# Performance work log

Hardware: AMD Instinct MI355X
Metric: run time of the kernel (lower is better)

Reference implementation:

```python
import jax, jax.numpy as jnp
import numpy as np

EPS = 1e-6
DATA_DIM = 2048
LATENT_DIM = 64
ENC = [1024, 1024, 2048]
BATCH = 8192
K_ROUNDS = 24  # fixed proposal rounds for Marsaglia-Tsang rejection (accept prob per round > 0.95)


def _sample_gamma_boosted(key, al, be):
    """Marsaglia-Tsang sampler with alpha-boost, matching the torch al<1 branch.

    Samples Gamma(al+1, 1) via squeeze/rejection, then applies the
    u^(1/al) boost and divides by be, exactly as:
    exp(log(d*v + 1e-6) + log(u + 1e-6)/(al + 1e-6)) / (be + 1e-6)
    """
    d = (al + 1.0) - 1.0 / 3.0              # [B, L]
    c = 1.0 / jnp.sqrt(9.0 * d)             # [B, L]
    k1, k2 = jax.random.split(key)
    eps = jax.random.normal(k1, (K_ROUNDS,) + al.shape, dtype=al.dtype)
    u = jax.random.uniform(k2, (K_ROUNDS,) + al.shape, dtype=al.dtype,
                           minval=1e-7, maxval=1.0)
    v = 1.0 + c[None] * eps                 # [K, B, L]
    v3 = v * v * v
    safe_v3 = jnp.where(v > 0, v3, 1.0)
    # squeeze accept OR full log-accept (standard MT test, as in source index1/index2)
    accept = (v > 0) & ((u < 1.0 - 0.0331 * (eps * eps) * (eps * eps)) |
                        (jnp.log(u) < 0.5 * eps * eps + d[None] * (1.0 - safe_v3 + jnp.log(safe_v3))))
    idx = jnp.argmax(accept, axis=0)        # first accepted round per element
    eps_s = jnp.take_along_axis(eps, idx[None], axis=0)[0]
    u_s = jnp.take_along_axis(u, idx[None], axis=0)[0]
    v_s = (1.0 + c * eps_s) ** 3
    return jnp.exp(jnp.log(d * v_s + EPS) + jnp.log(u_s + EPS) / (al + EPS)) / (be + EPS)


def setup_inputs() -> dict:
    key = jax.random.key(0)
    ks = jax.random.split(key, 20)

    def lin(k, fan_in, fan_out):
        kw, kb = jax.random.split(k)
        w = jax.random.normal(kw, (fan_in, fan_out), dtype=jnp.float32) / np.sqrt(fan_in)
        b = jax.random.normal(kb, (fan_out,), dtype=jnp.float32) * 0.01
        return w, b

    inp = {"x": jax.random.uniform(ks[0], (BATCH, DATA_DIM), dtype=jnp.float32)}
    inp["fc1_w"], inp["fc1_b"] = lin(ks[1], DATA_DIM, ENC[0])
    inp["fc2_w"], inp["fc2_b"] = lin(ks[2], ENC[0], ENC[1])
    inp["fc3_w"], inp["fc3_b"] = lin(ks[3], ENC[1], ENC[2])
    inp["fc41_w"], inp["fc41_b"] = lin(ks[4], ENC[2], LATENT_DIM)
    inp["fc42_w"], inp["fc42_b"] = lin(ks[5], ENC[2], LATENT_DIM)
    inp["fc4_w"], inp["fc4_b"] = lin(ks[6], LATENT_DIM, ENC[2])
    inp["fc5_w"], inp["fc5_b"] = lin(ks[7], ENC[2], ENC[1])
    inp["fc6_w"], inp["fc6_b"] = lin(ks[8], ENC[1], ENC[0])
    inp["fc7_w"], inp["fc7_b"] = lin(ks[9], ENC[0], DATA_DIM * 2)
    return inp


def reference(x, fc1_w, fc1_b, fc2_w, fc2_b, fc3_w, fc3_b,
              fc41_w, fc41_b, fc42_w, fc42_b,
              fc4_w, fc4_b, fc5_w, fc5_b, fc6_w, fc6_b, fc7_w, fc7_b):
    relu, sp = jax.nn.relu, jax.nn.softplus
    # encoder
    h1 = relu(x @ fc1_w + fc1_b)
    h2 = relu(h1 @ fc2_w + fc2_b)
    h3 = relu(h2 @ fc3_w + fc3_b)
    logalpha = EPS + sp(h3 @ fc41_w + fc41_b)   # [B, L], positive
    logbeta = EPS + sp(h3 @ fc42_w + fc42_b)
    # reparameterize via Marsaglia-Tsang gamma rejection sampling
    z = _sample_gamma_boosted(jax.random.key(42), logalpha, logbeta)
    # decoder (torch calls decode(z) twice with identical result; compute once)
    h4 = relu(z @ fc4_w + fc4_b)
    h5 = relu(h4 @ fc5_w + fc5_b)
    h6 = relu(h5 @ fc6_w + fc6_b)
    dec = h6 @ fc7_w + fc7_b                    # [B, 2*DATA_DIM]
    recon_al = EPS + sp(dec[:, :DATA_DIM])
    recon_be = EPS + sp(dec[:, DATA_DIM:])
    return (recon_al, recon_be, logalpha, logbeta, z)
```

## Files before the change

kernel.cpp:

```cpp
#include <hip/hip_runtime.h>
#include <stdint.h>

#define DEVFN static __device__ __forceinline__

typedef __attribute__((ext_vector_type(8))) short short8;
typedef __attribute__((ext_vector_type(4))) float floatx4;
typedef _Float16 half8 __attribute__((ext_vector_type(8)));

DEVFN uint32_t rotl32(uint32_t v, int d) { return (v << d) | (v >> (32 - d)); }

DEVFN void tf2x32(uint32_t k0, uint32_t k1, uint32_t x0, uint32_t x1,
                  uint32_t& o0, uint32_t& o1) {
  uint32_t k2 = k0 ^ k1 ^ 0x1BD11BDAu;
  x0 += k0; x1 += k1;
  x0 += x1; x1 = rotl32(x1, 13); x1 ^= x0;
  x0 += x1; x1 = rotl32(x1, 15); x1 ^= x0;
  x0 += x1; x1 = rotl32(x1, 26); x1 ^= x0;
  x0 += x1; x1 = rotl32(x1, 6);  x1 ^= x0;
  x0 += k1; x1 += k2 + 1u;
  x0 += x1; x1 = rotl32(x1, 17); x1 ^= x0;
  x0 += x1; x1 = rotl32(x1, 29); x1 ^= x0;
  x0 += x1; x1 = rotl32(x1, 16); x1 ^= x0;
  x0 += x1; x1 = rotl32(x1, 24); x1 ^= x0;
  x0 += k2; x1 += k0 + 2u;
  x0 += x1; x1 = rotl32(x1, 13); x1 ^= x0;
  x0 += x1; x1 = rotl32(x1, 15); x1 ^= x0;
  x0 += x1; x1 = rotl32(x1, 26); x1 ^= x0;
  x0 += x1; x1 = rotl32(x1, 6);  x1 ^= x0;
  x0 += k0; x1 += k1 + 3u;
  x0 += x1; x1 = rotl32(x1, 17); x1 ^= x0;
  x0 += x1; x1 = rotl32(x1, 29); x1 ^= x0;
  x0 += x1; x1 = rotl32(x1, 16); x1 ^= x0;
  x0 += x1; x1 = rotl32(x1, 24); x1 ^= x0;
  x0 += k1; x1 += k2 + 4u;
  x0 += x1; x1 = rotl32(x1, 13); x1 ^= x0;
  x0 += x1; x1 = rotl32(x1, 15); x1 ^= x0;
  x0 += x1; x1 = rotl32(x1, 26); x1 ^= x0;
  x0 += x1; x1 = rotl32(x1, 6);  x1 ^= x0;
  x0 += k2; x1 += k0 + 5u;
  o0 = x0; o1 = x1;
}

DEVFN float erfinv_f32(float x) {
#pragma clang fp contract(off)
  float w = -log1pf(-(x * x));
  float p;
  if (w < 5.0f) {
    w = w - 2.5f;
    p = 2.81022636e-08f;
    p = 3.43273939e-07f + p * w;
    p = -3.5233877e-06f + p * w;
    p = -4.39150654e-06f + p * w;
    p = 0.00021858087f + p * w;
    p = -0.00125372503f + p * w;
    p = -0.00417768164f + p * w;
    p = 0.246640727f + p * w;
    p = 1.50140941f + p * w;
  } else {
    w = __fsqrt_rn(w) - 3.0f;
    p = -0.000200214257f;
    p = 0.000100950558f + p * w;
    p = 0.00134934322f + p * w;
    p = -0.00367342844f + p * w;
    p = 0.00573950773f + p * w;
    p = -0.0076224613f + p * w;
    p = 0.00943887047f + p * w;
    p = 1.00167406f + p * w;
    p = 2.83297682f + p * w;
  }
  return p * x;
}

DEVFN float softplus_ref(float v) {
#pragma clang fp contract(off)
  return fmaxf(v, 0.0f) + log1pf(expf(-fabsf(v)));
}

DEVFN ushort f2bf(float f) {
  uint32_t u = __float_as_uint(f);
  uint32_t r = (u + 0x7FFFu + ((u >> 16) & 1u)) >> 16;
  return (ushort)r;
}

DEVFN void split2(float a, ushort& hb, ushort& lb) {
  _Float16 h = (_Float16)a;
  float r = (a - (float)h) * 2048.0f;
  _Float16 l = (_Float16)r;
  hb = __builtin_bit_cast(unsigned short, h);
  lb = __builtin_bit_cast(unsigned short, l);
}

DEVFN void gl2lds16(const void* g, void* l) {
  __builtin_amdgcn_global_load_lds(
      (const __attribute__((address_space(1))) void*)g,
      (__attribute__((address_space(3))) void*)l, 16, 0, 0);
}

__global__ __launch_bounds__(256) void split_f16(
    const float* __restrict__ in, ushort* __restrict__ oh,
    ushort* __restrict__ ol, int n4) {
  int idx = blockIdx.x * 256 + threadIdx.x;
  int stride = gridDim.x * 256;
  for (int i = idx; i < n4; i += stride) {
    float4 a = ((const float4*)in)[i];
    ushort h0, h1, h2, h3, l0, l1, l2, l3;
    split2(a.x, h0, l0); split2(a.y, h1, l1);
    split2(a.z, h2, l2); split2(a.w, h3, l3);
    ushort4 hv; hv.x = h0; hv.y = h1; hv.z = h2; hv.w = h3;
    ushort4 lv; lv.x = l0; lv.y = l1; lv.z = l2; lv.w = l3;
    ((ushort4*)oh)[i] = hv;
    ((ushort4*)ol)[i] = lv;
  }
}

__global__ __launch_bounds__(256) void transpose_split_f16(
    const float* __restrict__ in, ushort* __restrict__ oh,
    ushort* __restrict__ ol, int R, int C) {
  __shared__ float tile[32][33];
  const int c0 = blockIdx.x * 32, r0 = blockIdx.y * 32;
  const int tx = threadIdx.x & 31, ty = threadIdx.x >> 5;
#pragma unroll
  for (int i = ty; i < 32; i += 8)
    tile[i][tx] = in[(size_t)(r0 + i) * C + c0 + tx];
  __syncthreads();
#pragma unroll
  for (int i = ty; i < 32; i += 8) {
    ushort hb, lb;
    split2(tile[tx][i], hb, lb);
    size_t o = (size_t)(c0 + i) * R + r0 + tx;
    oh[o] = hb; ol[o] = lb;
  }
}

template <int ACT>
__global__ __launch_bounds__(256) void gemm_f16x3(
    const ushort* __restrict__ Ah, const ushort* __restrict__ Al,
    const ushort* __restrict__ Bh, const ushort* __restrict__ Bl,
    const float* __restrict__ bias, ushort* __restrict__ Oh,
    ushort* __restrict__ Ol, float* __restrict__ Of, int M, int N, int K) {
  __shared__ ushort AsH[128 * 32];
  __shared__ ushort AsL[128 * 32];
  __shared__ ushort BsH[128 * 32];
  __shared__ ushort BsL[128 * 32];
  const int tid = threadIdx.x;
  const int wave = tid >> 6, lane = tid & 63;
  const int m0 = blockIdx.y * 128, n0 = blockIdx.x * 128;
  const int lrow = lane & 15, lq = lane >> 4;
  const int wm = wave & 1, wn = wave >> 1;
  const int srow = lane >> 2;
  const int scol = (lane & 3) * 8;

  floatx4 acc1[4][4], acc2[4][4];
#pragma unroll
  for (int i = 0; i < 4; i++)
#pragma unroll
    for (int j = 0; j < 4; j++) {
      acc1[i][j] = (floatx4){0.f, 0.f, 0.f, 0.f};
      acc2[i][j] = (floatx4){0.f, 0.f, 0.f, 0.f};
    }

  for (int k0 = 0; k0 < K; k0 += 32) {
#pragma unroll
    for (int h = 0; h < 2; h++) {
      int r0 = wave * 32 + h * 16;
      gl2lds16(Ah + (size_t)(m0 + r0 + srow) * K + k0 + scol, &AsH[r0 * 32]);
      gl2lds16(Al + (size_t)(m0 + r0 + srow) * K + k0 + scol, &AsL[r0 * 32]);
      gl2lds16(Bh + (size_t)(n0 + r0 + srow) * K + k0 + scol, &BsH[r0 * 32]);
      gl2lds16(Bl + (size_t)(n0 + r0 + srow) * K + k0 + scol, &BsL[r0 * 32]);
    }
    __syncthreads();
    half8 ah[4], al[4];
#pragma unroll
    for (int i = 0; i < 4; i++) {
      ah[i] = *(const half8*)&AsH[(wm * 64 + i * 16 + lrow) * 32 + lq * 8];
      al[i] = *(const half8*)&AsL[(wm * 64 + i * 16 + lrow) * 32 + lq * 8];
    }
#pragma unroll
    for (int j = 0; j < 4; j++) {
      half8 bh = *(const half8*)&BsH[(wn * 64 + j * 16 + lrow) * 32 + lq * 8];
      half8 bl = *(const half8*)&BsL[(wn * 64 + j * 16 + lrow) * 32 + lq * 8];
#pragma unroll
      for (int i = 0; i < 4; i++) {
        acc1[i][j] = __builtin_amdgcn_mfma_f32_16x16x32_f16(ah[i], bh,
                                                            acc1[i][j], 0, 0, 0);
        acc2[i][j] = __builtin_amdgcn_mfma_f32_16x16x32_f16(ah[i], bl,
                                                            acc2[i][j], 0, 0, 0);
        acc2[i][j] = __builtin_amdgcn_mfma_f32_16x16x32_f16(al[i], bh,
                                                            acc2[i][j], 0, 0, 0);
      }
    }
    __syncthreads();
  }

  const float INV2048 = 4.8828125e-4f;
#pragma unroll
  for (int i = 0; i < 4; i++) {
#pragma unroll
    for (int j = 0; j < 4; j++) {
      int colg = n0 + wn * 64 + j * 16 + lrow;
      float bb = bias[colg];
#pragma unroll
      for (int r = 0; r < 4; r++) {
        int rowg = m0 + wm * 64 + i * 16 + lq * 4 + r;
        float v = acc1[i][j][r] + acc2[i][j][r] * INV2048 + bb;
        v = fmaxf(v, 0.0f);
        if (ACT == 1) {
          ushort hb, lb;
          split2(v, hb, lb);
          size_t o = (size_t)rowg * N + colg;
          Oh[o] = hb; Ol[o] = lb;
        } else {
          Of[(size_t)rowg * N + colg] = v;
        }
      }
    }
  }
}

__global__ __launch_bounds__(256) void dual_mfma(
    const ushort* __restrict__ Ah, const ushort* __restrict__ Al,
    const ushort* __restrict__ Bh, const ushort* __restrict__ Bl,
    float* __restrict__ P) {
  __shared__ ushort AsH[128 * 32];
  __shared__ ushort AsL[128 * 32];
  __shared__ ushort BsH[128 * 32];
  __shared__ ushort BsL[128 * 32];
  const int K = 2048;
  const int tid = threadIdx.x;
  const int wave = tid >> 6, lane = tid & 63;
  const int m0 = blockIdx.y * 128;
  const int kbase = blockIdx.x * 256;
  const int lrow = lane & 15, lq = lane >> 4;
  const int wm = wave & 1, wn = wave >> 1;
  const int srow = lane >> 2;
  const int scol = (lane & 3) * 8;

  floatx4 acc1[4][4], acc2[4][4];
#pragma unroll
  for (int i = 0; i < 4; i++)
#pragma unroll
    for (int j = 0; j < 4; j++) {
      acc1[i][j] = (floatx4){0.f, 0.f, 0.f, 0.f};
      acc2[i][j] = (floatx4){0.f, 0.f, 0.f, 0.f};
    }

  for (int kk = 0; kk < 256; kk += 32) {
    int k0 = kbase + kk;
#pragma unroll
    for (int h = 0; h < 2; h++) {
      int r0 = wave * 32 + h * 16;
      gl2lds16(Ah + (size_t)(m0 + r0 + srow) * K + k0 + scol, &AsH[r0 * 32]);
      gl2lds16(Al + (size_t)(m0 + r0 + srow) * K + k0 + scol, &AsL[r0 * 32]);
      gl2lds16(Bh + (size_t)(r0 + srow) * K + k0 + scol, &BsH[r0 * 32]);
      gl2lds16(Bl + (size_t)(r0 + srow) * K + k0 + scol, &BsL[r0 * 32]);
    }
    __syncthreads();
    half8 ah[4], al[4];
#pragma unroll
    for (int i = 0; i < 4; i++) {
      ah[i] = *(const half8*)&AsH[(wm * 64 + i * 16 + lrow) * 32 + lq * 8];
      al[i] = *(const half8*)&AsL[(wm * 64 + i * 16 + lrow) * 32 + lq * 8];
    }
#pragma unroll
    for (int j = 0; j < 4; j++) {
      half8 bh = *(const half8*)&BsH[(wn * 64 + j * 16 + lrow) * 32 + lq * 8];
      half8 bl = *(const half8*)&BsL[(wn * 64 + j * 16 + lrow) * 32 + lq * 8];
#pragma unroll
      for (int i = 0; i < 4; i++) {
        acc1[i][j] = __builtin_amdgcn_mfma_f32_16x16x32_f16(ah[i], bh,
                                                            acc1[i][j], 0, 0, 0);
        acc2[i][j] = __builtin_amdgcn_mfma_f32_16x16x32_f16(ah[i], bl,
                                                            acc2[i][j], 0, 0, 0);
        acc2[i][j] = __builtin_amdgcn_mfma_f32_16x16x32_f16(al[i], bh,
                                                            acc2[i][j], 0, 0, 0);
      }
    }
    __syncthreads();
  }

  const float INV2048 = 4.8828125e-4f;
#pragma unroll
  for (int i = 0; i < 4; i++) {
#pragma unroll
    for (int j = 0; j < 4; j++) {
      int colg = wn * 64 + j * 16 + lrow;
#pragma unroll
      for (int r = 0; r < 4; r++) {
        int rowg = m0 + wm * 64 + i * 16 + lq * 4 + r;
        float v = acc1[i][j][r] + acc2[i][j][r] * INV2048;
        P[((size_t)blockIdx.x * 8192 + rowg) * 128 + colg] = v;
      }
    }
  }
}

__global__ __launch_bounds__(256) void dual_reduce(
    const float* __restrict__ P, const float* __restrict__ b41,
    const float* __restrict__ b42, float* __restrict__ la,
    float* __restrict__ lb) {
#pragma clang fp contract(off)
  int idx = blockIdx.x * 256 + threadIdx.x;
  int row = idx >> 5;
  int c4 = (idx & 31) * 4;
  float4 s = {0.f, 0.f, 0.f, 0.f};
#pragma unroll
  for (int k = 0; k < 8; k++) {
    float4 p = *(const float4*)&P[((size_t)k * 8192 + row) * 128 + c4];
    s.x += p.x; s.y += p.y; s.z += p.z; s.w += p.w;
  }
  float o[4];
  const float* bb = (c4 < 64) ? (b41 + c4) : (b42 + c4 - 64);
#pragma unroll
  for (int q = 0; q < 4; q++) {
    float v = (&s.x)[q] + bb[q];
    o[q] = 1e-6f + softplus_ref(v);
  }
  float* dst = (c4 < 64) ? (la + (size_t)row * 64 + c4)
                         : (lb + (size_t)row * 64 + (c4 - 64));
  *(float4*)dst = *(float4*)o;
}

__global__ __launch_bounds__(256) void gamma_sampler(
    const float* __restrict__ la, const float* __restrict__ lb,
    float* __restrict__ z, ushort* __restrict__ zb) {
#pragma clang fp contract(off)
  const uint32_t i = blockIdx.x * 256u + threadIdx.x;
  uint32_t k1a, k1b, k2a, k2b;
  tf2x32(0u, 42u, 0u, 0u, k1a, k1b);
  tf2x32(0u, 42u, 0u, 1u, k2a, k2b);

  const float LO = __uint_as_float(0xBF7FFFFFu);
  const float SQRT2 = __uint_as_float(0x3FB504F3u);
  const float USCALE = 1.0f - 1e-7f;

  const float al = la[i];
  const float be = lb[i];
  const float d = (al + 1.0f) - 0.33333334f;
  const float c = 1.0f / __fsqrt_rn(9.0f * d);

  float es = 0.0f, us = 0.0f;
  bool done = false;
  for (int k = 0; k < 24; k++) {
    if (__all(done)) break;
    if (!done) {
      uint32_t n = (uint32_t)k * 524288u + i;
      uint32_t o0, o1, p0, p1;
      tf2x32(k1a, k1b, 0u, n, o0, o1);
      tf2x32(k2a, k2b, 0u, n, p0, p1);
      uint32_t eb = o0 ^ o1;
      uint32_t ub = p0 ^ p1;
      float f = __uint_as_float((eb >> 9) | 0x3F800000u) - 1.0f;
      float un = f * 2.0f + LO;
      un = fmaxf(LO, un);
      float e = SQRT2 * erfinv_f32(un);
      float g = __uint_as_float((ub >> 9) | 0x3F800000u) - 1.0f;
      float u = g * USCALE + 1e-7f;
      u = fmaxf(1e-7f, u);
      if (k == 0) { es = e; us = u; }
      float v = 1.0f + c * e;
      if (v > 0.0f) {
        float v3 = (v * v) * v;
        float e2 = e * e;
        bool acc = false;
        float sq = 1.0f - (0.0331f * e2) * e2;
        if (u < sq) acc = true;
        else {
          float rhs = (0.5f * e) * e + d * ((1.0f - v3) + logf(v3));
          if (logf(u) < rhs) acc = true;
        }
        if (acc) { es = e; us = u; done = true; }
      }
    }
  }
  float vv = 1.0f + c * es;
  float vs = (vv * vv) * vv;
  float t = logf(d * vs + 1e-6f) + logf(us + 1e-6f) / (al + 1e-6f);
  float zv = expf(t) / (be + 1e-6f);
  z[i] = zv;
  zb[i] = f2bf(zv);
}

__global__ __launch_bounds__(256) void transpose_bf16(
    const float* __restrict__ in, ushort* __restrict__ out, int R, int C) {
  __shared__ float tile[32][33];
  const int c0 = blockIdx.x * 32, r0 = blockIdx.y * 32;
  const int tx = threadIdx.x & 31, ty = threadIdx.x >> 5;
#pragma unroll
  for (int i = ty; i < 32; i += 8)
    tile[i][tx] = in[(size_t)(r0 + i) * C + c0 + tx];
  __syncthreads();
#pragma unroll
  for (int i = ty; i < 32; i += 8)
    out[(size_t)(c0 + i) * R + r0 + tx] = f2bf(tile[tx][i]);
}

template <int ACT>
__global__ __launch_bounds__(256) void gemm_bf16(
    const ushort* __restrict__ A, const ushort* __restrict__ Bt,
    const float* __restrict__ bias, ushort* __restrict__ C0b,
    float* __restrict__ C0f, float* __restrict__ C1f,
    int M, int N, int K, int split) {
  __shared__ ushort As[128 * 32];
  __shared__ ushort Bs[128 * 32];
  const int tid = threadIdx.x;
  const int wave = tid >> 6, lane = tid & 63;
  const int m0 = blockIdx.y * 128, n0 = blockIdx.x * 128;
  const int lrow = lane & 15, lq = lane >> 4;
  const int wm = wave & 1, wn = wave >> 1;
  const int srow = lane >> 2;
  const int scol = (lane & 3) * 8;

  floatx4 acc[4][4];
#pragma unroll
  for (int i = 0; i < 4; i++)
#pragma unroll
    for (int j = 0; j < 4; j++) acc[i][j] = (floatx4){0.f, 0.f, 0.f, 0.f};

  for (int k0 = 0; k0 < K; k0 += 32) {
#pragma unroll
    for (int h = 0; h < 2; h++) {
      int r0 = wave * 32 + h * 16;
      gl2lds16(A + (size_t)(m0 + r0 + srow) * K + k0 + scol, &As[r0 * 32]);
      gl2lds16(Bt + (size_t)(n0 + r0 + srow) * K + k0 + scol, &Bs[r0 * 32]);
    }
    __syncthreads();
    short8 a[4], b[4];
#pragma unroll
    for (int i = 0; i < 4; i++) {
      a[i] = *(const short8*)&As[(wm * 64 + i * 16 + lrow) * 32 + lq * 8];
      b[i] = *(const short8*)&Bs[(wn * 64 + i * 16 + lrow) * 32 + lq * 8];
    }
#pragma unroll
    for (int i = 0; i < 4; i++)
#pragma unroll
      for (int j = 0; j < 4; j++)
        acc[i][j] = __builtin_amdgcn_mfma_f32_16x16x32_bf16(a[i], b[j],
                                                            acc[i][j], 0, 0, 0);
    __syncthreads();
  }

#pragma unroll
  for (int i = 0; i < 4; i++) {
#pragma unroll
    for (int j = 0; j < 4; j++) {
      int colg = n0 + wn * 64 + j * 16 + lrow;
      float bb = bias[colg];
#pragma unroll
      for (int r = 0; r < 4; r++) {
        int rowg = m0 + wm * 64 + i * 16 + lq * 4 + r;
        float v = acc[i][j][r] + bb;
        if (ACT == 0) {
          v = fmaxf(v, 0.0f);
          C0b[(size_t)rowg * N + colg] = f2bf(v);
        } else {
          v = 1e-6f + softplus_ref(v);
          if (colg < split) C0f[(size_t)rowg * split + colg] = v;
          else              C1f[(size_t)rowg * split + (colg - split)] = v;
        }
      }
    }
  }
}

extern "C" void kernel_launch(void* const* d_in, const int* in_sizes, int n_in,
                              void* d_out, int out_size, void* d_ws,
                              size_t ws_size, hipStream_t stream) {
  const float* x   = (const float*)d_in[0];
  const float* w1  = (const float*)d_in[1];  const float* b1  = (const float*)d_in[2];
  const float* w2  = (const float*)d_in[3];  const float* b2  = (const float*)d_in[4];
  const float* w3  = (const float*)d_in[5];  const float* b3  = (const float*)d_in[6];
  const float* w41 = (const float*)d_in[7];  const float* b41 = (const float*)d_in[8];
  const float* w42 = (const float*)d_in[9];  const float* b42 = (const float*)d_in[10];
  const float* w4  = (const float*)d_in[11]; const float* b4  = (const float*)d_in[12];
  const float* w5  = (const float*)d_in[13]; const float* b5  = (const float*)d_in[14];
  const float* w6  = (const float*)d_in[15]; const float* b6  = (const float*)d_in[16];
  const float* w7  = (const float*)d_in[17]; const float* b7  = (const float*)d_in[18];
  float* out = (float*)d_out;
  float* ws  = (float*)d_ws;
  ushort* wsu = (ushort*)d_ws;

  float* recon_a = out;
  float* recon_b = out + 16777216;
  float* la      = out + 33554432;
  float* lb      = out + 34078720;
  float* zz      = out + 34603008;

  ushort* xh   = wsu;
  ushort* xl   = wsu + 16777216;
  ushort* w1Th = wsu + 33554432;
  ushort* w1Tl = wsu + 35651584;
  ushort* w2Th = wsu + 37748736;
  ushort* w2Tl = wsu + 38797312;
  ushort* h1h  = wsu + 39845888;
  ushort* h1l  = wsu + 48234496;
  ushort* w3Th = wsu + 16777216;
  ushort* w3Tl = wsu + 18874368;
  ushort* h2h  = wsu;
  ushort* h2l  = wsu + 8388608;
  ushort* h3h  = wsu + 20971520;
  ushort* h3l  = wsu + 37748736;
  ushort* wcatTh = wsu + 16777216;
  ushort* wcatTl = wsu + 17039360;
  float*  Ppart = ws;
  ushort* w4T = wsu + 54525952;
  ushort* w5T = wsu + 54657024;
  ushort* w6T = wsu + 56754176;
  ushort* w7T = wsu + 57802752;
  ushort* zb  = wsu;
  ushort* h4b = wsu + 20971520;
  ushort* h5b = wsu + 524288;
  ushort* h6b = wsu + 8912896;

  dim3 blk(256);
  split_f16<<<dim3(2048), blk, 0, stream>>>(x, xh, xl, 4194304);
  transpose_split_f16<<<dim3(32, 64), blk, 0, stream>>>(w1, w1Th, w1Tl, 2048, 1024);
  transpose_split_f16<<<dim3(32, 32), blk, 0, stream>>>(w2, w2Th, w2Tl, 1024, 1024);
  gemm_f16x3<1><<<dim3(8, 64), blk, 0, stream>>>(xh, xl, w1Th, w1Tl, b1,
                                                 h1h, h1l, nullptr, 8192, 1024, 2048);
  transpose_split_f16<<<dim3(64, 32), blk, 0, stream>>>(w3, w3Th, w3Tl, 1024, 2048);
  gemm_f16x3<1><<<dim3(8, 64), blk, 0, stream>>>(h1h, h1l, w2Th, w2Tl, b2,
                                                 h2h, h2l, nullptr, 8192, 1024, 1024);
  transpose_bf16<<<dim3(64, 2),   blk, 0, stream>>>(w4, w4T, 64,   2048);
  transpose_bf16<<<dim3(32, 64),  blk, 0, stream>>>(w5, w5T, 2048, 1024);
  transpose_bf16<<<dim3(32, 32),  blk, 0, stream>>>(w6, w6T, 1024, 1024);
  transpose_bf16<<<dim3(128, 32), blk, 0, stream>>>(w7, w7T, 1024, 4096);
  gemm_f16x3<1><<<dim3(16, 64), blk, 0, stream>>>(h2h, h2l, w3Th, w3Tl, b3,
                                                  h3h, h3l, nullptr, 8192, 2048, 1024);
  transpose_split_f16<<<dim3(2, 64), blk, 0, stream>>>(w41, wcatTh, wcatTl, 2048, 64);
  transpose_split_f16<<<dim3(2, 64), blk, 0, stream>>>(w42, wcatTh + 64 * 2048,
                                                       wcatTl + 64 * 2048, 2048, 64);
  dual_mfma<<<dim3(8, 64), blk, 0, stream>>>(h3h, h3l, wcatTh, wcatTl, Ppart);
  dual_reduce<<<dim3(1024), blk, 0, stream>>>(Ppart, b41, b42, la, lb);
  gamma_sampler<<<dim3(2048), blk, 0, stream>>>(la, lb, zz, zb);
  gemm_bf16<0><<<dim3(16, 64), blk, 0, stream>>>(zb,  w4T, b4, h4b, nullptr, nullptr, 8192, 2048, 64, 0);
  gemm_bf16<0><<<dim3(8, 64),  blk, 0, stream>>>(h4b, w5T, b5, h5b, nullptr, nullptr, 8192, 1024, 2048, 0);
  gemm_bf16<0><<<dim3(8, 64),  blk, 0, stream>>>(h5b, w6T, b6, h6b, nullptr, nullptr, 8192, 1024, 1024, 0);
  gemm_bf16<3><<<dim3(32, 64), blk, 0, stream>>>(h6b, w7T, b7, nullptr, recon_a, recon_b, 8192, 4096, 1024, 2048);
  (void)in_sizes; (void)n_in; (void)out_size; (void)ws_size;
}
```

Baseline: 1.077 ms.

## Double-buffer LDS tiles in both GEMMs, add XCD block swizzle, fast softplus

Both GEMM kernels now keep two LDS buffers per operand and prefetch the next K-tile with global_load_lds while MFMAs run on the current one, so each iteration needs one barrier instead of two. Block indices are remapped so consecutive tiles land on the same XCD, which should improve L2 reuse. The decoder-output softplus switches to the __expf/__logf intrinsics, trading some accuracy for fewer instructions. Doubling LDS use may reduce the number of resident blocks per CU.

```diff
diff --git a/kernel.cpp b/kernel.cpp
--- a/kernel.cpp
+++ b/kernel.cpp
@@ -76,6 +76,11 @@
   return fmaxf(v, 0.0f) + log1pf(expf(-fabsf(v)));
 }
 
+DEVFN float softplus_fast(float v) {
+  float e = __expf(-fabsf(v));
+  return fmaxf(v, 0.0f) + __logf(1.0f + e);
+}
+
 DEVFN ushort f2bf(float f) {
   uint32_t u = __float_as_uint(f);
   uint32_t r = (u + 0x7FFFu + ((u >> 16) & 1u)) >> 16;
@@ -94,6 +99,11 @@
   __builtin_amdgcn_global_load_lds(
       (const __attribute__((address_space(1))) void*)g,
       (__attribute__((address_space(3))) void*)l, 16, 0, 0);
+}
+
+DEVFN int xcd_swizzle(int bid, int nwg) {
+  if ((nwg & 7) == 0) return (bid & 7) * (nwg >> 3) + (bid >> 3);
+  return bid;
 }
 
 __global__ __launch_bounds__(256) void split_f16(
@@ -138,13 +148,15 @@
     const ushort* __restrict__ Bh, const ushort* __restrict__ Bl,
     const float* __restrict__ bias, ushort* __restrict__ Oh,
     ushort* __restrict__ Ol, float* __restrict__ Of, int M, int N, int K) {
-  __shared__ ushort AsH[128 * 32];
-  __shared__ ushort AsL[128 * 32];
-  __shared__ ushort BsH[128 * 32];
-  __shared__ ushort BsL[128 * 32];
+  __shared__ ushort AsH[2][128 * 32];
+  __shared__ ushort AsL[2][128 * 32];
+  __shared__ ushort BsH[2][128 * 32];
+  __shared__ ushort BsL[2][128 * 32];
   const int tid = threadIdx.x;
   const int wave = tid >> 6, lane = tid & 63;
-  const int m0 = blockIdx.y * 128, n0 = blockIdx.x * 128;
+  const int nbx = gridDim.x;
+  const int bid = xcd_swizzle(blockIdx.y * nbx + blockIdx.x, nbx * gridDim.y);
+  const int m0 = (bid / nbx) * 128, n0 = (bid % nbx) * 128;
   const int lrow = lane & 15, lq = lane >> 4;
   const int wm = wave & 1, wn = wave >> 1;
   const int srow = lane >> 2;
@@ -159,26 +171,34 @@
       acc2[i][j] = (floatx4){0.f, 0.f, 0.f, 0.f};
     }
 
-  for (int k0 = 0; k0 < K; k0 += 32) {
+  auto stage = [&](int k0, int pp) {
 #pragma unroll
     for (int h = 0; h < 2; h++) {
       int r0 = wave * 32 + h * 16;
-      gl2lds16(Ah + (size_t)(m0 + r0 + srow) * K + k0 + scol, &AsH[r0 * 32]);
-      gl2lds16(Al + (size_t)(m0 + r0 + srow) * K + k0 + scol, &AsL[r0 * 32]);
-      gl2lds16(Bh + (size_t)(n0 + r0 + srow) * K + k0 + scol, &BsH[r0 * 32]);
-      gl2lds16(Bl + (size_t)(n0 + r0 + srow) * K + k0 + scol, &BsL[r0 * 32]);
-    }
-    __syncthreads();
+      gl2lds16(Ah + (size_t)(m0 + r0 + srow) * K + k0 + scol, &AsH[pp][r0 * 32]);
+      gl2lds16(Al + (size_t)(m0 + r0 + srow) * K + k0 + scol, &AsL[pp][r0 * 32]);
+      gl2lds16(Bh + (size_t)(n0 + r0 + srow) * K + k0 + scol, &BsH[pp][r0 * 32]);
+      gl2lds16(Bl + (size_t)(n0 + r0 + srow) * K + k0 + scol, &BsL[pp][r0 * 32]);
+    }
+  };
+
+  const int nt = K >> 5;
+  stage(0, 0);
+  asm volatile("s_waitcnt vmcnt(0)" ::: "memory");
+  __builtin_amdgcn_s_barrier();
+  int cur = 0;
+  for (int t = 0; t < nt; t++) {
+    if (t + 1 < nt) stage((t + 1) << 5, cur ^ 1);
     half8 ah[4], al[4];
 #pragma unroll
     for (int i = 0; i < 4; i++) {
-      ah[i] = *(const half8*)&AsH[(wm * 64 + i * 16 + lrow) * 32 + lq * 8];
-      al[i] = *(const half8*)&AsL[(wm * 64 + i * 16 + lrow) * 32 + lq * 8];
-    }
-#pragma unroll
-    for (int j = 0; j < 4; j++) {
-      half8 bh = *(const half8*)&BsH[(wn * 64 + j * 16 + lrow) * 32 + lq * 8];
-      half8 bl = *(const half8*)&BsL[(wn * 64 + j * 16 + lrow) * 32 + lq * 8];
+      ah[i] = *(const half8*)&AsH[cur][(wm * 64 + i * 16 + lrow) * 32 + lq * 8];
+      al[i] = *(const half8*)&AsL[cur][(wm * 64 + i * 16 + lrow) * 32 + lq * 8];
+    }
+#pragma unroll
+    for (int j = 0; j < 4; j++) {
+      half8 bh = *(const half8*)&BsH[cur][(wn * 64 + j * 16 + lrow) * 32 + lq * 8];
+      half8 bl = *(const half8*)&BsL[cur][(wn * 64 + j * 16 + lrow) * 32 + lq * 8];
 #pragma unroll
       for (int i = 0; i < 4; i++) {
         acc1[i][j] = __builtin_amdgcn_mfma_f32_16x16x32_f16(ah[i], bh,
@@ -189,7 +209,10 @@
                                                             acc2[i][j], 0, 0, 0);
       }
     }
-    __syncthreads();
+    asm volatile("s_waitcnt vmcnt(0)" ::: "memory");
+    __builtin_amdgcn_sched_barrier(0);
+    __builtin_amdgcn_s_barrier();
+    cur ^= 1;
   }
 
   const float INV2048 = 4.8828125e-4f;
@@ -400,11 +423,13 @@
     const float* __restrict__ bias, ushort* __restrict__ C0b,
     float* __restrict__ C0f, float* __restrict__ C1f,
     int M, int N, int K, int split) {
-  __shared__ ushort As[128 * 32];
-  __shared__ ushort Bs[128 * 32];
+  __shared__ ushort As[2][128 * 32];
+  __shared__ ushort Bs[2][128 * 32];
   const int tid = threadIdx.x;
   const int wave = tid >> 6, lane = tid & 63;
-  const int m0 = blockIdx.y * 128, n0 = blockIdx.x * 128;
+  const int nbx = gridDim.x;
+  const int bid = xcd_swizzle(blockIdx.y * nbx + blockIdx.x, nbx * gridDim.y);
+  const int m0 = (bid / nbx) * 128, n0 = (bid % nbx) * 128;
   const int lrow = lane & 15, lq = lane >> 4;
   const int wm = wave & 1, wn = wave >> 1;
   const int srow = lane >> 2;
@@ -416,19 +441,27 @@
 #pragma unroll
     for (int j = 0; j < 4; j++) acc[i][j] = (floatx4){0.f, 0.f, 0.f, 0.f};
 
-  for (int k0 = 0; k0 < K; k0 += 32) {
+  auto stage = [&](int k0, int pp) {
 #pragma unroll
     for (int h = 0; h < 2; h++) {
       int r0 = wave * 32 + h * 16;
-      gl2lds16(A + (size_t)(m0 + r0 + srow) * K + k0 + scol, &As[r0 * 32]);
-      gl2lds16(Bt + (size_t)(n0 + r0 + srow) * K + k0 + scol, &Bs[r0 * 32]);
-    }
-    __syncthreads();
+      gl2lds16(A + (size_t)(m0 + r0 + srow) * K + k0 + scol, &As[pp][r0 * 32]);
+      gl2lds16(Bt + (size_t)(n0 + r0 + srow) * K + k0 + scol, &Bs[pp][r0 * 32]);
+    }
+  };
+
+  const int nt = K >> 5;
+  stage(0, 0);
+  asm volatile("s_waitcnt vmcnt(0)" ::: "memory");
+  __builtin_amdgcn_s_barrier();
+  int cur = 0;
+  for (int t = 0; t < nt; t++) {
+    if (t + 1 < nt) stage((t + 1) << 5, cur ^ 1);
     short8 a[4], b[4];
 #pragma unroll
     for (int i = 0; i < 4; i++) {
-      a[i] = *(const short8*)&As[(wm * 64 + i * 16 + lrow) * 32 + lq * 8];
-      b[i] = *(const short8*)&Bs[(wn * 64 + i * 16 + lrow) * 32 + lq * 8];
+      a[i] = *(const short8*)&As[cur][(wm * 64 + i * 16 + lrow) * 32 + lq * 8];
+      b[i] = *(const short8*)&Bs[cur][(wn * 64 + i * 16 + lrow) * 32 + lq * 8];
     }
 #pragma unroll
     for (int i = 0; i < 4; i++)
@@ -436,7 +469,10 @@
       for (int j = 0; j < 4; j++)
         acc[i][j] = __builtin_amdgcn_mfma_f32_16x16x32_bf16(a[i], b[j],
                                                             acc[i][j], 0, 0, 0);
-    __syncthreads();
+    asm volatile("s_waitcnt vmcnt(0)" ::: "memory");
+    __builtin_amdgcn_sched_barrier(0);
+    __builtin_amdgcn_s_barrier();
+    cur ^= 1;
   }
 
 #pragma unroll
@@ -453,7 +489,7 @@
           v = fmaxf(v, 0.0f);
           C0b[(size_t)rowg * N + colg] = f2bf(v);
         } else {
-          v = 1e-6f + softplus_ref(v);
+          v = 1e-6f + softplus_fast(v);
           if (colg < split) C0f[(size_t)rowg * split + colg] = v;
           else              C1f[(size_t)rowg * split + (colg - split)] = v;
         }
```

Measured after the change: 922.1 us. 1.17x faster.
